# Kernel tuning notes

Hardware: AMD Instinct MI355X
Metric: run time of the kernel (lower is better)

Reference implementation:

```python
import jax, jax.numpy as jnp
from jax import lax
import numpy as np

T, B = 64, 32          # timesteps, n_envs
C_IN, HW = 4, 64
H_LSTM = 256
FEAT = 64 * 4 * 4      # conv output flattened (1024)
FC = 512


def _conv(x, w, b, stride):
    # x: [N,C,H,W], w: [O,I,kh,kw] (torch OIHW), VALID padding like nn.Conv2d default
    y = lax.conv_general_dilated(x, w, (stride, stride), 'VALID',
                                 dimension_numbers=('NCHW', 'OIHW', 'NCHW'))
    return y + b[None, :, None, None]


def setup_inputs() -> dict:
    key = jax.random.key(0)
    ks = jax.random.split(key, 16)
    s = lambda *sh: sh
    d = {
        'x': jax.random.uniform(ks[0], (T * B, C_IN, HW, HW), jnp.float32) * 255.0,
        'done': jax.random.randint(ks[1], (T * B,), 0, 2, jnp.int32),
        'conv1_w': jax.random.normal(ks[2], (32, C_IN, 8, 8), jnp.float32) * 0.05,
        'conv1_b': jnp.zeros((32,), jnp.float32),
        'conv2_w': jax.random.normal(ks[3], (64, 32, 4, 4), jnp.float32) * 0.05,
        'conv2_b': jnp.zeros((64,), jnp.float32),
        'conv3_w': jax.random.normal(ks[4], (64, 64, 3, 3), jnp.float32) * 0.05,
        'conv3_b': jnp.zeros((64,), jnp.float32),
        'fc_w': jax.random.normal(ks[5], (FC, FEAT), jnp.float32) * 0.02,
        'fc_b': jnp.zeros((FC,), jnp.float32),
        'w_ih': jax.random.normal(ks[6], (4 * H_LSTM, FC), jnp.float32) * 0.03,
        'w_hh': jax.random.normal(ks[7], (4 * H_LSTM, H_LSTM), jnp.float32) * 0.03,
        'b_ih': jnp.zeros((4 * H_LSTM,), jnp.float32),
        'b_hh': jnp.zeros((4 * H_LSTM,), jnp.float32),
        'h0': jnp.zeros((1, B, H_LSTM), jnp.float32),
        'c0': jnp.zeros((1, B, H_LSTM), jnp.float32),
    }
    return d


def reference(x, done, conv1_w, conv1_b, conv2_w, conv2_b, conv3_w, conv3_b,
              fc_w, fc_b, w_ih, w_hh, b_ih, b_hh, h0, c0):
    # CNN encoder on x/255
    z = x / 255.0
    z = jax.nn.relu(_conv(z, conv1_w, conv1_b, 4))   # [TB,32,15,15]
    z = jax.nn.relu(_conv(z, conv2_w, conv2_b, 2))   # [TB,64,6,6]
    z = jax.nn.relu(_conv(z, conv3_w, conv3_b, 1))   # [TB,64,4,4]
    z = z.reshape(z.shape[0], -1)                    # [TB,1024]
    feats = jax.nn.relu(z @ fc_w.T + fc_b)           # [TB,512]

    n_envs = h0.shape[1]
    feats = feats.reshape(-1, n_envs, feats.shape[1])        # [T,B,512]
    mask = (1.0 - done.astype(feats.dtype)).reshape(-1, n_envs)  # [T,B]

    H = h0.shape[-1]

    def step(carry, inp):
        h, c = carry                    # [B,H] each
        f_t, m_t = inp                  # [B,512], [B]
        m = m_t[:, None]
        h = h * m
        c = c * m
        gates = f_t @ w_ih.T + b_ih + h @ w_hh.T + b_hh   # [B,4H]
        i, f, g, o = jnp.split(gates, 4, axis=-1)         # torch order: i,f,g,o
        c = jax.nn.sigmoid(f) * c + jax.nn.sigmoid(i) * jnp.tanh(g)
        h = jax.nn.sigmoid(o) * jnp.tanh(c)
        return (h, c), h

    (_, _), hs = lax.scan(step, (h0[0], c0[0]), (feats, mask))  # hs: [T,B,H]
    return hs.reshape(-1, H)   # [T*B, H]
```

## Files before the change

kernel.cpp:

```cpp
#include <hip/hip_runtime.h>
#include <math.h>


#define NIMG 2048

typedef _Float16 half2_t __attribute__((ext_vector_type(2)));
typedef __fp16 fp16x2_t __attribute__((ext_vector_type(2)));

__device__ inline unsigned short f2h_bits(float f) {
    union { _Float16 h; unsigned short u; } x;
    x.h = (_Float16)f;
    return x.u;
}

__device__ inline unsigned pack2_rne(float a, float b) {
    return (unsigned)f2h_bits(a) | ((unsigned)f2h_bits(b) << 16);
}

__device__ inline unsigned pack2_fast(float a, float b) {
#if __has_builtin(__builtin_amdgcn_cvt_pkrtz)
    union { fp16x2_t h; unsigned u; } x;
    x.h = __builtin_amdgcn_cvt_pkrtz(a, b);
    return x.u;
#else
    return pack2_rne(a, b);
#endif
}

__device__ inline float dot2(unsigned hu, unsigned wu, float acc) {
    union { unsigned u; half2_t h; } a, b;
    a.u = hu; b.u = wu;
#if __has_builtin(__builtin_amdgcn_fdot2)
    return __builtin_amdgcn_fdot2(a.h, b.h, acc, false);
#else
    return acc + (float)a.h.x * (float)b.h.x + (float)a.h.y * (float)b.h.y;
#endif
}

__device__ inline float fast_tanh(float x) {
    return 1.0f - 2.0f / (__expf(2.0f * x) + 1.0f);
}

__global__ void pack_all_kernel(const float* __restrict__ whh,
                                const float* __restrict__ w1,
                                const float* __restrict__ w2,
                                const float* __restrict__ w3,
                                const float* __restrict__ fcw,
                                const float* __restrict__ wih,
                                unsigned* __restrict__ wp,
                                unsigned* __restrict__ w1p,
                                unsigned* __restrict__ w2p,
                                unsigned* __restrict__ w3ph,
                                unsigned* __restrict__ fcwph,
                                unsigned* __restrict__ wihph) {
    int idx = blockIdx.x * 256 + threadIdx.x;
    if (idx < 131072) {
        int d4 = idx >> 12, rem = idx & 4095, row = rem >> 2, j = idx & 3;
        const float* s = whh + (size_t)row * 256 + d4 * 8 + j * 2;
        wp[idx] = pack2_rne(s[0], s[1]);
        return;
    }
    idx -= 131072;
    if (idx < 4096) {
        int oc = idx >> 7, rem = idx & 127;
        int ic = rem >> 5, ky = (rem >> 2) & 7, kxp = rem & 3;
        const float* s = w1 + (((size_t)oc * 4 + ic) * 8 + ky) * 8 + kxp * 2;
        w1p[idx] = pack2_rne(s[0], s[1]);
        return;
    }
    idx -= 4096;
    if (idx < 16384) {
        int p = idx >> 6, oc = idx & 63;
        int ic = p >> 3, ky = (p >> 1) & 3, kxp = p & 1;
        const float* s = w2 + (size_t)oc * 512 + ic * 16 + ky * 4 + kxp * 2;
        w2p[idx] = pack2_rne(s[0], s[1]);
        return;
    }
    idx -= 16384;
    if (idx < 18432) {
        int oc = idx & 63, rest = idx >> 6;
        int icp = rest & 31, kxy = rest >> 5;
        int ky = kxy / 3, kx = kxy - ky * 3;
        const float* s = w3 + (((size_t)oc * 64 + icp * 2) * 3 + ky) * 3 + kx;
        w3ph[idx] = pack2_rne(s[0], s[9]);
        return;
    }
    idx -= 18432;
    if (idx < 262144) {
        const float* s = fcw + (size_t)idx * 2;
        fcwph[idx] = pack2_rne(s[0], s[1]);
        return;
    }
    idx -= 262144;
    if (idx < 262144) {
        const float* s = wih + (size_t)idx * 2;
        wihph[idx] = pack2_rne(s[0], s[1]);
    }
}

__global__ __launch_bounds__(1024) void conv1_kernel(const float* __restrict__ x,
                                                     const unsigned* __restrict__ w1p,
                                                     const float* __restrict__ b,
                                                     unsigned short* __restrict__ z1) {
    __shared__ unsigned short xs[4 * 64 * 64];
    int n = blockIdx.x;
    int tid = threadIdx.x;
    const float* xp = x + (size_t)n * 16384;
    const float inv = 1.0f / 255.0f;
    for (int i = tid * 4; i < 16384; i += 4096) {
        float4 v = *(const float4*)(xp + i);
        uint2 q;
        q.x = pack2_fast(v.x * inv, v.y * inv);
        q.y = pack2_fast(v.z * inv, v.w * inv);
        *(uint2*)&xs[i] = q;
    }
    __syncthreads();
    int lane = tid & 63, wave = tid >> 6;
    int gg = __builtin_amdgcn_readfirstlane(wave & 3);
    int pos = (wave >> 2) * 64 + lane;
    if (pos < 225) {
        int oy = pos / 15, ox = pos - oy * 15;
        float acc[8];
        const float* bp = b + gg * 8;
#pragma unroll
        for (int u = 0; u < 8; ++u) acc[u] = bp[u];
        for (int ic = 0; ic < 4; ++ic) {
            uint2 qa[8], qb[8];
#pragma unroll
            for (int ky = 0; ky < 8; ++ky) {
                const unsigned short* row = &xs[(ic * 64 + oy * 4 + ky) * 64 + ox * 4];
                qa[ky] = *(const uint2*)row;
                qb[ky] = *(const uint2*)(row + 4);
            }
#pragma unroll
            for (int ky = 0; ky < 8; ++ky) {
                const unsigned* wpt = w1p + ((((gg * 8) * 4 + ic) * 8 + ky) * 4);
#pragma unroll
                for (int u = 0; u < 8; ++u) {
                    const unsigned* wu = wpt + u * 128;
                    acc[u] = dot2(qa[ky].x, wu[0], acc[u]);
                    acc[u] = dot2(qa[ky].y, wu[1], acc[u]);
                    acc[u] = dot2(qb[ky].x, wu[2], acc[u]);
                    acc[u] = dot2(qb[ky].y, wu[3], acc[u]);
                }
            }
        }
        unsigned short* op = z1 + (size_t)n * 7680 + (gg * 8) * 240 + oy * 16 + ox;
#pragma unroll
        for (int u = 0; u < 8; ++u) op[u * 240] = f2h_bits(fmaxf(acc[u], 0.0f));
    }
}

__global__ __launch_bounds__(768) void conv2_kernel(const unsigned short* __restrict__ z1,
                                                    const unsigned* __restrict__ w2p,
                                                    const float* __restrict__ bias,
                                                    unsigned* __restrict__ z2h) {
    __shared__ unsigned short xs[2][32 * 15 * 16];
    int tid = threadIdx.x;
    int n0 = blockIdx.x * 2;
#pragma unroll
    for (int img = 0; img < 2; ++img) {
        const unsigned* src = (const unsigned*)(z1 + (size_t)(n0 + img) * 7680);
        unsigned* dst = (unsigned*)xs[img];
        for (int i = tid; i < 3840; i += 768) dst[i] = src[i];
    }
    __syncthreads();
    int lane = tid & 63, wave = tid >> 6;
    int img = wave / 6;
    int oy = wave - img * 6;
    int n = n0 + img;
    float bv = bias[lane];
    float acc[6];
#pragma unroll
    for (int u = 0; u < 6; ++u) acc[u] = bv;
    for (int ic = 0; ic < 32; ++ic) {
        uint4 ra[4], rb[4];
        unsigned wa[4], wb[4];
#pragma unroll
        for (int ky = 0; ky < 4; ++ky) {
            const unsigned short* row = &xs[img][(ic * 15 + oy * 2 + ky) * 16];
            ra[ky] = *(const uint4*)row;
            rb[ky] = *(const uint4*)(row + 8);
            const unsigned* wpp = w2p + ((ic * 4 + ky) * 2) * 64 + lane;
            wa[ky] = wpp[0];
            wb[ky] = wpp[64];
        }
#pragma unroll
        for (int ky = 0; ky < 4; ++ky) {
            unsigned p[8] = {ra[ky].x, ra[ky].y, ra[ky].z, ra[ky].w,
                             rb[ky].x, rb[ky].y, rb[ky].z, rb[ky].w};
#pragma unroll
            for (int u = 0; u < 6; ++u) {
                acc[u] = dot2(p[u], wa[ky], acc[u]);
                acc[u] = dot2(p[u + 1], wb[ky], acc[u]);
            }
        }
    }
    unsigned* zb = z2h + (size_t)n * 1152;
#pragma unroll
    for (int u = 0; u < 6; ++u) {
        float a = fmaxf(acc[u], 0.0f);
        float a2 = __shfl_xor(a, 1);
        if ((lane & 1) == 0) {
            zb[(oy * 6 + u) * 32 + (lane >> 1)] = pack2_rne(a, a2);
        }
    }
}

__global__ __launch_bounds__(512) void conv3_kernel(const unsigned* __restrict__ z2h,
                                                    const unsigned* __restrict__ w3ph,
                                                    const float* __restrict__ bias,
                                                    unsigned* __restrict__ outp) {
    __shared__ unsigned w3s[18432];
    __shared__ unsigned xs8[8][1152];
    int tid = threadIdx.x;
    int n0 = blockIdx.x * 8;
    for (int i = tid; i < 18432; i += 512) w3s[i] = w3ph[i];
    for (int i = tid; i < 8 * 1152; i += 512) {
        int img = i / 1152;
        int rem = i - img * 1152;
        int pos = rem >> 5, icp = rem & 31;
        xs8[img][icp * 36 + pos] = z2h[(size_t)(n0 + img) * 1152 + rem];
    }
    __syncthreads();
    int lane = tid & 63, img = tid >> 6;
    int n = n0 + img;
    float bv = bias[lane];
    float acc[4][4];
#pragma unroll
    for (int oy = 0; oy < 4; ++oy)
#pragma unroll
        for (int ox = 0; ox < 4; ++ox) acc[oy][ox] = bv;
    const unsigned* wb = w3s + lane;
    const unsigned* xb = xs8[img];
    for (int icp = 0; icp < 32; ++icp) {
        unsigned xr[36];
#pragma unroll
        for (int p4 = 0; p4 < 9; ++p4)
            *(uint4*)&xr[p4 * 4] = *(const uint4*)&xb[icp * 36 + p4 * 4];
        unsigned wv[9];
#pragma unroll
        for (int k9 = 0; k9 < 9; ++k9)
            wv[k9] = wb[(k9 * 32 + icp) * 64];
#pragma unroll
        for (int ky = 0; ky < 3; ++ky)
#pragma unroll
            for (int kx = 0; kx < 3; ++kx) {
                unsigned w = wv[ky * 3 + kx];
#pragma unroll
                for (int oy = 0; oy < 4; ++oy)
#pragma unroll
                    for (int ox = 0; ox < 4; ++ox)
                        acc[oy][ox] = dot2(xr[(oy + ky) * 6 + ox + kx], w, acc[oy][ox]);
            }
    }
    unsigned* op = outp + (size_t)n * 512 + lane * 8;
#pragma unroll
    for (int oy = 0; oy < 4; ++oy) {
        float a0 = fmaxf(acc[oy][0], 0.f), a1 = fmaxf(acc[oy][1], 0.f);
        float a2 = fmaxf(acc[oy][2], 0.f), a3 = fmaxf(acc[oy][3], 0.f);
        op[oy * 2 + 0] = pack2_rne(a0, a1);
        op[oy * 2 + 1] = pack2_rne(a2, a3);
    }
}

__global__ __launch_bounds__(256) void gemm_bt_h(const unsigned* __restrict__ A,
                                                 const unsigned* __restrict__ B,
                                                 const float* __restrict__ bias,
                                                 const float* __restrict__ bias2,
                                                 float* __restrict__ C,
                                                 unsigned* __restrict__ Ch,
                                                 int M, int N, int Kp, int relu) {
    __shared__ unsigned As[16][66];
    __shared__ unsigned Bs[16][66];
    int tid = threadIdx.x;
    int m0 = blockIdx.y * 64, n0 = blockIdx.x * 64;
    int tx = tid & 15, ty = tid >> 4;
    int lr = tid >> 2;
    int lk = (tid & 3) * 4;
    const unsigned* Ap = A + (size_t)(m0 + lr) * Kp + lk;
    const unsigned* Bp = B + (size_t)(n0 + lr) * Kp + lk;
    float acc[4][4];
#pragma unroll
    for (int i = 0; i < 4; ++i)
#pragma unroll
        for (int j = 0; j < 4; ++j) acc[i][j] = 0.0f;

    uint4 av = *(const uint4*)Ap;
    uint4 bv = *(const uint4*)Bp;
    for (int k0 = 0; k0 < Kp; k0 += 16) {
        __syncthreads();
        As[lk + 0][lr] = av.x;
        As[lk + 1][lr] = av.y;
        As[lk + 2][lr] = av.z;
        As[lk + 3][lr] = av.w;
        Bs[lk + 0][lr] = bv.x;
        Bs[lk + 1][lr] = bv.y;
        Bs[lk + 2][lr] = bv.z;
        Bs[lk + 3][lr] = bv.w;
        __syncthreads();
        if (k0 + 16 < Kp) {
            av = *(const uint4*)(Ap + k0 + 16);
            bv = *(const uint4*)(Bp + k0 + 16);
        }
#pragma unroll
        for (int kk = 0; kk < 16; ++kk) {
            unsigned a[4], b[4];
            *(uint4*)a = *(const uint4*)&As[kk][ty * 4];
            *(uint4*)b = *(const uint4*)&Bs[kk][tx * 4];
#pragma unroll
            for (int i = 0; i < 4; ++i)
#pragma unroll
                for (int j = 0; j < 4; ++j) acc[i][j] = dot2(a[i], b[j], acc[i][j]);
        }
    }
    float bb[4];
#pragma unroll
    for (int j = 0; j < 4; ++j) {
        float v = bias[n0 + tx * 4 + j];
        if (bias2) v += bias2[n0 + tx * 4 + j];
        bb[j] = v;
    }
#pragma unroll
    for (int i = 0; i < 4; ++i) {
        float4 o;
        o.x = acc[i][0] + bb[0];
        o.y = acc[i][1] + bb[1];
        o.z = acc[i][2] + bb[2];
        o.w = acc[i][3] + bb[3];
        if (relu) {
            o.x = fmaxf(o.x, 0.0f);
            o.y = fmaxf(o.y, 0.0f);
            o.z = fmaxf(o.z, 0.0f);
            o.w = fmaxf(o.w, 0.0f);
        }
        size_t mrow = (size_t)(m0 + ty * 4 + i);
        if (C) *(float4*)&C[mrow * N + n0 + tx * 4] = o;
        if (Ch) {
            unsigned* cp = Ch + mrow * (N >> 1) + (n0 >> 1) + tx * 2;
            cp[0] = pack2_rne(o.x, o.y);
            cp[1] = pack2_rne(o.z, o.w);
        }
    }
}

__global__ __launch_bounds__(1024) void lstm_kernel(const float* __restrict__ gi,
                                                    const unsigned* __restrict__ wp,
                                                    const int* __restrict__ done,
                                                    const float* __restrict__ h0,
                                                    const float* __restrict__ c0,
                                                    float* __restrict__ out) {
    __shared__ alignas(16) unsigned wo[32768];
    __shared__ alignas(16) unsigned h2u[128];
    __shared__ float xch[4096];
    int b = blockIdx.x, tt = threadIdx.x;
    int u = tt & 255, q = tt >> 8;
    int q8 = q * 8;

    const uint4* wsrc = (const uint4*)wp;

    {
        uint4* dst = (uint4*)wo;
        for (int i4 = tt; i4 < 8192; i4 += 1024) {
            int d4 = i4 >> 8, r = i4 & 255;
            dst[i4] = wsrc[d4 * 1024 + 768 + r];
        }
    }

#define LDW(j)                                              \
    uint4 wi##j = wsrc[(q8 + j) * 1024 + u];                \
    uint4 wf##j = wsrc[(q8 + j) * 1024 + 256 + u];          \
    uint4 wg##j = wsrc[(q8 + j) * 1024 + 512 + u];
    LDW(0) LDW(1) LDW(2) LDW(3) LDW(4) LDW(5) LDW(6) LDW(7)
#undef LDW

    if (tt < 128) {
        h2u[tt] = pack2_rne(h0[b * 256 + 2 * tt], h0[b * 256 + 2 * tt + 1]);
    }
    float c = 0.0f;
    float gv0 = 0.f, gv1 = 0.f, gv2 = 0.f, gv3 = 0.f;
    int dn = done[b];
    const float* gbase = gi + (size_t)b * 1024;
    if (q == 0) {
        c = c0[b * 256 + u];
        gv0 = gbase[u];
        gv1 = gbase[256 + u];
        gv2 = gbase[512 + u];
        gv3 = gbase[768 + u];
    }
    __syncthreads();

    const uint4* h2u4 = (const uint4*)h2u;
    const uint4* wo4 = (const uint4*)wo;

    for (int step = 0; step < 64; ++step) {
        int dnn = 0;
        if (step < 63) dnn = done[(step + 1) * 32 + b];
        float nx0 = 0.f, nx1 = 0.f, nx2 = 0.f, nx3 = 0.f;
        if (q == 0 && step < 63) {
            const float* gb = gbase + (size_t)(step + 1) * 32768;
            nx0 = gb[u];
            nx1 = gb[256 + u];
            nx2 = gb[512 + u];
            nx3 = gb[768 + u];
        }

        float pI = 0.f, pF = 0.f, pG = 0.f, pO = 0.f;
        if (!dn) {
#define MV(j) {                                                         \
        uint4 ha = h2u4[q8 + j];          \
        uint4 wv = wo4[(q8 + j) * 256 + u];   \
        pI = dot2(ha.x, wi##j.x, pI); pI = dot2(ha.y, wi##j.y, pI);     \
        pI = dot2(ha.z, wi##j.z, pI); pI = dot2(ha.w, wi##j.w, pI);     \
        pF = dot2(ha.x, wf##j.x, pF); pF = dot2(ha.y, wf##j.y, pF);     \
        pF = dot2(ha.z, wf##j.z, pF); pF = dot2(ha.w, wf##j.w, pF);     \
        pG = dot2(ha.x, wg##j.x, pG); pG = dot2(ha.y, wg##j.y, pG);     \
        pG = dot2(ha.z, wg##j.z, pG); pG = dot2(ha.w, wg##j.w, pG);     \
        pO = dot2(ha.x, wv.x, pO);    pO = dot2(ha.y, wv.y, pO);        \
        pO = dot2(ha.z, wv.z, pO);    pO = dot2(ha.w, wv.w, pO); }
            MV(0) MV(1) MV(2) MV(3) MV(4) MV(5) MV(6) MV(7)
#undef MV
        }

        xch[q * 1024 + u] = pI;
        xch[q * 1024 + 256 + u] = pF;
        xch[q * 1024 + 512 + u] = pG;
        xch[q * 1024 + 768 + u] = pO;
        __syncthreads();

        if (q == 0) {
            float m = 1.0f - (float)dn;
            float sI = xch[u] + xch[1024 + u] + xch[2048 + u] + xch[3072 + u];
            float sF = xch[256 + u] + xch[1280 + u] + xch[2304 + u] + xch[3328 + u];
            float sG = xch[512 + u] + xch[1536 + u] + xch[2560 + u] + xch[3584 + u];
            float sO = xch[768 + u] + xch[1792 + u] + xch[2816 + u] + xch[3840 + u];
            float g_i = gv0 + m * sI;
            float g_f = gv1 + m * sF;
            float g_g = gv2 + m * sG;
            float g_o = gv3 + m * sO;
            float si = 1.0f / (1.0f + __expf(-g_i));
            float sf = 1.0f / (1.0f + __expf(-g_f));
            float so = 1.0f / (1.0f + __expf(-g_o));
            float tg = fast_tanh(g_g);
            c = sf * (c * m) + si * tg;
            float hn = so * fast_tanh(c);
            out[((size_t)step * 32 + b) * 256 + u] = hn;
            float hn2 = __shfl_xor(hn, 1);
            if ((u & 1) == 0) {
                unsigned lo = f2h_bits(hn);
                unsigned hi = f2h_bits(hn2);
                h2u[u >> 1] = lo | (hi << 16);
            }
        }
        __syncthreads();

        gv0 = nx0; gv1 = nx1; gv2 = nx2; gv3 = nx3;
        dn = dnn;
    }
}

extern "C" void kernel_launch(void* const* d_in, const int* in_sizes, int n_in,
                              void* d_out, int out_size, void* d_ws, size_t ws_size,
                              hipStream_t stream) {
    const float* x    = (const float*)d_in[0];
    const int*   done = (const int*)d_in[1];
    const float* w1   = (const float*)d_in[2];
    const float* b1   = (const float*)d_in[3];
    const float* w2   = (const float*)d_in[4];
    const float* b2   = (const float*)d_in[5];
    const float* w3   = (const float*)d_in[6];
    const float* b3   = (const float*)d_in[7];
    const float* fcw  = (const float*)d_in[8];
    const float* fcb  = (const float*)d_in[9];
    const float* wih  = (const float*)d_in[10];
    const float* whh  = (const float*)d_in[11];
    const float* bih  = (const float*)d_in[12];
    const float* bhh  = (const float*)d_in[13];
    const float* h0   = (const float*)d_in[14];
    const float* c0   = (const float*)d_in[15];
    float* out = (float*)d_out;
    float* ws = (float*)d_ws;

    unsigned short* z1u = (unsigned short*)(ws + 0);
    unsigned* z2h = (unsigned*)(ws + 8000000);
    unsigned* z3h = (unsigned*)(ws + 0);
    unsigned* featsh = (unsigned*)(ws + 2097152);
    float* gi     = ws + 3145728;
    unsigned* fcwph = (unsigned*)(ws + 10400000);
    unsigned* wihph = (unsigned*)(ws + 10700000);
    unsigned* w3ph  = (unsigned*)(ws + 13000000);
    unsigned* w1p = (unsigned*)(ws + 13100000);
    unsigned* w2p = (unsigned*)(ws + 13200000);
    unsigned* wp  = (unsigned*)(ws + 13300000);

    pack_all_kernel<<<(694272 + 255) / 256, 256, 0, stream>>>(
        whh, w1, w2, w3, fcw, wih, wp, w1p, w2p, w3ph, fcwph, wihph);

    conv1_kernel<<<NIMG, 1024, 0, stream>>>(x, w1p, b1, z1u);
    conv2_kernel<<<NIMG / 2, 768, 0, stream>>>(z1u, w2p, b2, z2h);
    conv3_kernel<<<NIMG / 8, 512, 0, stream>>>(z2h, w3ph, b3, z3h);

    gemm_bt_h<<<dim3(512 / 64, NIMG / 64), 256, 0, stream>>>(
        z3h, fcwph, fcb, nullptr, nullptr, featsh, NIMG, 512, 512, 1);
    gemm_bt_h<<<dim3(1024 / 64, NIMG / 64), 256, 0, stream>>>(
        featsh, wihph, bih, bhh, gi, nullptr, NIMG, 1024, 256, 0);

    lstm_kernel<<<32, 1024, 0, stream>>>(gi, wp, done, h0, c0, out);
}
```

Measured before the change: 508.1 us.

## Pack conv1 output as vector stores, batch GEMM LDS reads, skip LSTM matvec on done

```diff
diff --git a/kernel.cpp b/kernel.cpp
--- a/kernel.cpp
+++ b/kernel.cpp
@@ -101,7 +101,7 @@
 __global__ __launch_bounds__(1024) void conv1_kernel(const float* __restrict__ x,
                                                      const unsigned* __restrict__ w1p,
                                                      const float* __restrict__ b,
-                                                     unsigned short* __restrict__ z1) {
+                                                     unsigned* __restrict__ z1p) {
     __shared__ unsigned short xs[4 * 64 * 64];
     int n = blockIdx.x;
     int tid = threadIdx.x;
@@ -145,24 +145,39 @@
                 }
             }
         }
-        unsigned short* op = z1 + (size_t)n * 7680 + (gg * 8) * 240 + oy * 16 + ox;
-#pragma unroll
-        for (int u = 0; u < 8; ++u) op[u * 240] = f2h_bits(fmaxf(acc[u], 0.0f));
-    }
-}
-
-__global__ __launch_bounds__(768) void conv2_kernel(const unsigned short* __restrict__ z1,
+        float r0 = fmaxf(acc[0], 0.f), r1 = fmaxf(acc[1], 0.f);
+        float r2 = fmaxf(acc[2], 0.f), r3 = fmaxf(acc[3], 0.f);
+        float r4 = fmaxf(acc[4], 0.f), r5 = fmaxf(acc[5], 0.f);
+        float r6 = fmaxf(acc[6], 0.f), r7 = fmaxf(acc[7], 0.f);
+        uint4 o;
+        o.x = pack2_rne(r0, r1);
+        o.y = pack2_rne(r2, r3);
+        o.z = pack2_rne(r4, r5);
+        o.w = pack2_rne(r6, r7);
+        *(uint4*)(z1p + (size_t)n * 3600 + gg * 900 + pos * 4) = o;
+    }
+}
+
+__global__ __launch_bounds__(768) void conv2_kernel(const unsigned* __restrict__ z1p,
                                                     const unsigned* __restrict__ w2p,
                                                     const float* __restrict__ bias,
                                                     unsigned* __restrict__ z2h) {
     __shared__ unsigned short xs[2][32 * 15 * 16];
     int tid = threadIdx.x;
     int n0 = blockIdx.x * 2;
-#pragma unroll
-    for (int img = 0; img < 2; ++img) {
-        const unsigned* src = (const unsigned*)(z1 + (size_t)(n0 + img) * 7680);
-        unsigned* dst = (unsigned*)xs[img];
-        for (int i = tid; i < 3840; i += 768) dst[i] = src[i];
+    for (int idx = tid; idx < 7200; idx += 768) {
+        int img = idx / 3600;
+        int r = idx - img * 3600;
+        int gg = r / 900;
+        int r2 = r - gg * 900;
+        int j = r2 / 225;
+        int pos = r2 - j * 225;
+        unsigned d = z1p[(size_t)(n0 + img) * 3600 + gg * 900 + pos * 4 + j];
+        int oc0 = gg * 8 + j * 2;
+        int row = pos / 15;
+        int col = pos - row * 15;
+        xs[img][(oc0 * 15 + row) * 16 + col] = (unsigned short)d;
+        xs[img][((oc0 + 1) * 15 + row) * 16 + col] = (unsigned short)(d >> 16);
     }
     __syncthreads();
     int lane = tid & 63, wave = tid >> 6;
@@ -304,14 +319,23 @@
             bv = *(const uint4*)(Bp + k0 + 16);
         }
 #pragma unroll
-        for (int kk = 0; kk < 16; ++kk) {
-            unsigned a[4], b[4];
-            *(uint4*)a = *(const uint4*)&As[kk][ty * 4];
-            *(uint4*)b = *(const uint4*)&Bs[kk][tx * 4];
-#pragma unroll
-            for (int i = 0; i < 4; ++i)
-#pragma unroll
-                for (int j = 0; j < 4; ++j) acc[i][j] = dot2(a[i], b[j], acc[i][j]);
+        for (int kk = 0; kk < 16; kk += 4) {
+            uint4 aF[4], bF[4];
+#pragma unroll
+            for (int t = 0; t < 4; ++t) {
+                aF[t] = *(const uint4*)&As[kk + t][ty * 4];
+                bF[t] = *(const uint4*)&Bs[kk + t][tx * 4];
+            }
+#pragma unroll
+            for (int t = 0; t < 4; ++t) {
+                unsigned a[4] = {aF[t].x, aF[t].y, aF[t].z, aF[t].w};
+                unsigned b[4] = {bF[t].x, bF[t].y, bF[t].z, bF[t].w};
+#pragma unroll
+                for (int i = 0; i < 4; ++i)
+#pragma unroll
+                    for (int j = 0; j < 4; ++j)
+                        acc[i][j] = dot2(a[i], b[j], acc[i][j]);
+            }
         }
     }
     float bb[4];
@@ -405,8 +429,8 @@
             nx3 = gb[768 + u];
         }
 
-        float pI = 0.f, pF = 0.f, pG = 0.f, pO = 0.f;
         if (!dn) {
+            float pI = 0.f, pF = 0.f, pG = 0.f, pO = 0.f;
 #define MV(j) {                                                         \
         uint4 ha = h2u4[q8 + j];          \
         uint4 wv = wo4[(q8 + j) * 256 + u];   \
@@ -420,39 +444,51 @@
         pO = dot2(ha.z, wv.z, pO);    pO = dot2(ha.w, wv.w, pO); }
             MV(0) MV(1) MV(2) MV(3) MV(4) MV(5) MV(6) MV(7)
 #undef MV
-        }
-
-        xch[q * 1024 + u] = pI;
-        xch[q * 1024 + 256 + u] = pF;
-        xch[q * 1024 + 512 + u] = pG;
-        xch[q * 1024 + 768 + u] = pO;
-        __syncthreads();
-
-        if (q == 0) {
-            float m = 1.0f - (float)dn;
-            float sI = xch[u] + xch[1024 + u] + xch[2048 + u] + xch[3072 + u];
-            float sF = xch[256 + u] + xch[1280 + u] + xch[2304 + u] + xch[3328 + u];
-            float sG = xch[512 + u] + xch[1536 + u] + xch[2560 + u] + xch[3584 + u];
-            float sO = xch[768 + u] + xch[1792 + u] + xch[2816 + u] + xch[3840 + u];
-            float g_i = gv0 + m * sI;
-            float g_f = gv1 + m * sF;
-            float g_g = gv2 + m * sG;
-            float g_o = gv3 + m * sO;
-            float si = 1.0f / (1.0f + __expf(-g_i));
-            float sf = 1.0f / (1.0f + __expf(-g_f));
-            float so = 1.0f / (1.0f + __expf(-g_o));
-            float tg = fast_tanh(g_g);
-            c = sf * (c * m) + si * tg;
-            float hn = so * fast_tanh(c);
-            out[((size_t)step * 32 + b) * 256 + u] = hn;
-            float hn2 = __shfl_xor(hn, 1);
-            if ((u & 1) == 0) {
-                unsigned lo = f2h_bits(hn);
-                unsigned hi = f2h_bits(hn2);
-                h2u[u >> 1] = lo | (hi << 16);
-            }
-        }
-        __syncthreads();
+            xch[q * 1024 + u] = pI;
+            xch[q * 1024 + 256 + u] = pF;
+            xch[q * 1024 + 512 + u] = pG;
+            xch[q * 1024 + 768 + u] = pO;
+            __syncthreads();
+
+            if (q == 0) {
+                float sI = xch[u] + xch[1024 + u] + xch[2048 + u] + xch[3072 + u];
+                float sF = xch[256 + u] + xch[1280 + u] + xch[2304 + u] + xch[3328 + u];
+                float sG = xch[512 + u] + xch[1536 + u] + xch[2560 + u] + xch[3584 + u];
+                float sO = xch[768 + u] + xch[1792 + u] + xch[2816 + u] + xch[3840 + u];
+                float g_i = gv0 + sI;
+                float g_f = gv1 + sF;
+                float g_g = gv2 + sG;
+                float g_o = gv3 + sO;
+                float si = 1.0f / (1.0f + __expf(-g_i));
+                float sf = 1.0f / (1.0f + __expf(-g_f));
+                float so = 1.0f / (1.0f + __expf(-g_o));
+                float tg = fast_tanh(g_g);
+                c = sf * c + si * tg;
+                float hn = so * fast_tanh(c);
+                out[((size_t)step * 32 + b) * 256 + u] = hn;
+                float hn2 = __shfl_xor(hn, 1);
+                if ((u & 1) == 0) {
+                    h2u[u >> 1] = (unsigned)f2h_bits(hn) |
+                                  ((unsigned)f2h_bits(hn2) << 16);
+                }
+            }
+            __syncthreads();
+        } else {
+            if (q == 0) {
+                float si = 1.0f / (1.0f + __expf(-gv0));
+                float so = 1.0f / (1.0f + __expf(-gv3));
+                float tg = fast_tanh(gv2);
+                c = si * tg;
+                float hn = so * fast_tanh(c);
+                out[((size_t)step * 32 + b) * 256 + u] = hn;
+                float hn2 = __shfl_xor(hn, 1);
+                if ((u & 1) == 0) {
+                    h2u[u >> 1] = (unsigned)f2h_bits(hn) |
+                                  ((unsigned)f2h_bits(hn2) << 16);
+                }
+            }
+            __syncthreads();
+        }
 
         gv0 = nx0; gv1 = nx1; gv2 = nx2; gv3 = nx3;
         dn = dnn;
@@ -481,7 +517,7 @@
     float* out = (float*)d_out;
     float* ws = (float*)d_ws;
 
-    unsigned short* z1u = (unsigned short*)(ws + 0);
+    unsigned* z1p = (unsigned*)(ws + 0);
     unsigned* z2h = (unsigned*)(ws + 8000000);
     unsigned* z3h = (unsigned*)(ws + 0);
     unsigned* featsh = (unsigned*)(ws + 2097152);
@@ -496,8 +532,8 @@
     pack_all_kernel<<<(694272 + 255) / 256, 256, 0, stream>>>(
         whh, w1, w2, w3, fcw, wih, wp, w1p, w2p, w3ph, fcwph, wihph);
 
-    conv1_kernel<<<NIMG, 1024, 0, stream>>>(x, w1p, b1, z1u);
-    conv2_kernel<<<NIMG / 2, 768, 0, stream>>>(z1u, w2p, b2, z2h);
+    conv1_kernel<<<NIMG, 1024, 0, stream>>>(x, w1p, b1, z1p);
+    conv2_kernel<<<NIMG / 2, 768, 0, stream>>>(z1p, w2p, b2, z2h);
     conv3_kernel<<<NIMG / 8, 512, 0, stream>>>(z2h, w3ph, b3, z3h);
 
     gemm_bt_h<<<dim3(512 / 64, NIMG / 64), 256, 0, stream>>>(
```

Result: no change. 506.6 us (-0.3%).
